# Kernel optimization log

Hardware: AMD Instinct MI355X
Metric: run time of the kernel (lower is better)

The kernel has to match this reference:

```python
import jax, jax.numpy as jnp
import numpy as np

D_MODEL = 1024

def setup_inputs() -> dict:
    key = jax.random.key(0)
    ks = jax.random.split(key, 5)
    d = D_MODEL
    s = 1.0 / np.sqrt(d)
    x = jax.random.normal(ks[0], (4, 4096, d), dtype=jnp.float32)
    qkv_w = jax.random.normal(ks[1], (3 * d, d), dtype=jnp.float32) * s
    qkv_b = jax.random.normal(ks[2], (3 * d,), dtype=jnp.float32) * 0.01
    out_w = jax.random.normal(ks[3], (d, d), dtype=jnp.float32) * s
    out_b = jax.random.normal(ks[4], (d,), dtype=jnp.float32) * 0.01
    return {"x": x, "qkv_w": qkv_w, "qkv_b": qkv_b, "out_w": out_w, "out_b": out_b}

def reference(x, qkv_w, qkv_b, out_w, out_b):
    # x: [b, s, d]; Linear applies x @ W^T + b (torch convention)
    d_model = x.shape[-1]
    qkv = jnp.einsum('bsd,ed->bse', x, qkv_w) + qkv_b  # [b, s, 3d]
    q, k, v = jnp.split(qkv, 3, axis=-1)
    # full-attention branch (chunk_size is None): scores scaled by 1/sqrt(d_model)
    scores = jnp.einsum('bqd,bkd->bqk', q, k) / jnp.sqrt(jnp.float32(d_model))
    attn = jax.nn.softmax(scores, axis=-1)
    attn_out = jnp.einsum('bqk,bkd->bqd', attn, v)
    return jnp.einsum('bsd,ed->bse', attn_out, out_w) + out_b
```

## Files before the change

### kernel.cpp

```cpp
#include <hip/hip_runtime.h>
#include <hip/hip_bf16.h>

typedef __bf16 bf16x8 __attribute__((ext_vector_type(8)));
typedef float f32x4 __attribute__((ext_vector_type(4)));
typedef _Float16 h8 __attribute__((ext_vector_type(8)));
typedef unsigned short u16x8 __attribute__((ext_vector_type(8)));

__device__ inline unsigned short f2b(float x) {
    __hip_bfloat16 h = __float2bfloat16(x);
    return __builtin_bit_cast(unsigned short, h);
}

__device__ inline void gload16(const void* g, void* l) {
    __builtin_amdgcn_global_load_lds(
        (const __attribute__((address_space(1))) unsigned int*)g,
        (__attribute__((address_space(3))) unsigned int*)l, 16, 0, 0);
}

#define BAR  asm volatile("s_barrier" ::: "memory")
#define VMC(N) asm volatile("s_waitcnt vmcnt(" #N ")" ::: "memory")
#define LKM(N) asm volatile("s_waitcnt lgkmcnt(" #N ")")

#define RD_A(BASE, MO)                                                \
    af[0][0] = *(const bf16x8*)((BASE) + (MO) * 1024 + aoff0);        \
    af[0][1] = *(const bf16x8*)((BASE) + (MO) * 1024 + aoff1);        \
    af[1][0] = *(const bf16x8*)((BASE) + ((MO) + 1) * 1024 + aoff0);  \
    af[1][1] = *(const bf16x8*)((BASE) + ((MO) + 1) * 1024 + aoff1);

#define RD_B(BASE)                                                    \
    _Pragma("unroll")                                                 \
    for (int n_ = 0; n_ < 4; ++n_) {                                  \
        bfr[n_][0] = *(const bf16x8*)((BASE) + n_ * 1024 + aoff0);    \
        bfr[n_][1] = *(const bf16x8*)((BASE) + n_ * 1024 + aoff1);    \
    }

#define MFMA_Q(MO)                                                    \
    __builtin_amdgcn_s_setprio(1);                                    \
    _Pragma("unroll")                                                 \
    for (int kk_ = 0; kk_ < 2; ++kk_)                                 \
        _Pragma("unroll")                                             \
        for (int mi_ = 0; mi_ < 2; ++mi_)                             \
            _Pragma("unroll")                                         \
            for (int n_ = 0; n_ < 4; ++n_)                            \
                acc[(MO) + mi_][n_] =                                 \
                    __builtin_amdgcn_mfma_f32_16x16x32_bf16(          \
                        af[mi_][kk_], bfr[n_][kk_],                   \
                        acc[(MO) + mi_][n_], 0, 0, 0);                \
    __builtin_amdgcn_s_setprio(0);

template<int EPI, int SWZ>
__global__ __launch_bounds__(512, 2) void gemm_nt(
    const unsigned short* __restrict__ A, const unsigned short* __restrict__ B,
    long aZ, long bZ, int lda, int ldb, int K,
    const float* __restrict__ bias,
    void* __restrict__ C0, void* __restrict__ C1, void* __restrict__ C2,
    long cZ, int ldc, float scale, int gx, int gy)
{
    __shared__ __attribute__((aligned(16))) unsigned short lds[2][4][8192];

    int wgid;
    if (SWZ) {
        const int nwg = (int)gridDim.x;
        const int bid = (int)blockIdx.x;
        const int qch = nwg >> 3, rch = nwg & 7;
        const int xcd = bid & 7, idx = bid >> 3;
        wgid = (xcd < rch ? xcd * (qch + 1)
                          : rch * (qch + 1) + (xcd - rch) * qch) + idx;
    } else {
        wgid = (int)blockIdx.x;
    }
    const int bx = wgid % gx;
    const int rem = wgid / gx;
    const int by = rem % gy;
    const int z = rem / gy;

    const int t = threadIdx.x;
    const int lane = t & 63, wid = t >> 6;
    const int wr = wid >> 2, wc = wid & 3;
    const int tileM = by * 256, tileN = bx * 256;
    A += (size_t)z * aZ;
    B += (size_t)z * bZ;

    f32x4 acc[8][4] = {};

    const int l4 = lane & 15, qw = lane >> 4, sw = lane & 7;
    const int aoff0 = l4 * 64 + ((qw ^ sw) << 3);
    const int aoff1 = l4 * 64 + (((4 | qw) ^ sw) << 3);

    const unsigned short* aB0 = &lds[0][wr][0];
    const unsigned short* aB1 = &lds[1][wr][0];
    const unsigned short* bB0 = &lds[0][2 + (wc >> 1)][0] + (wc & 1) * 4096;
    const unsigned short* bB1 = &lds[1][2 + (wc >> 1)][0] + (wc & 1) * 4096;

    const int srow = t >> 3;
    const int sg = ((t ^ (t >> 3)) & 7) << 3;
    const unsigned short* Asrc = A + (size_t)(tileM + srow) * lda + sg;
    const unsigned short* Bsrc = B + (size_t)(tileN + srow) * ldb + sg;

    auto stageA = [&](int kt, int h) {
        char* dst = (char*)&lds[kt & 1][h][0] + wid * 1024;
        const unsigned short* s = Asrc + (size_t)(h * 128) * lda + kt * 64;
        gload16(s, dst);
        gload16(s + (size_t)64 * lda, dst + 8192);
    };
    auto stageB = [&](int kt, int h) {
        char* dst = (char*)&lds[kt & 1][2 + h][0] + wid * 1024;
        const unsigned short* s = Bsrc + (size_t)(h * 128) * ldb + kt * 64;
        gload16(s, dst);
        gload16(s + (size_t)64 * ldb, dst + 8192);
    };

    const int NT = K >> 6;
    const int NI = NT >> 1;

    stageA(0, 0); stageA(0, 1); stageB(0, 0); stageB(0, 1);
    stageB(1, 0); stageB(1, 1);
    VMC(4);
    BAR;

    bf16x8 af[2][2], bfr[4][2];

#pragma unroll 1
    for (int i = 0; i < NI; ++i) {
        const int e = 2 * i, o = e + 1;
        const bool more = (i + 1 < NI);

        RD_B(bB0); RD_A(aB0, 0);
        stageA(o, 0);
        LKM(8);
        BAR; LKM(0); MFMA_Q(0); BAR;

        RD_A(aB0, 2);
        stageA(o, 1);
        BAR; LKM(0); MFMA_Q(2); BAR;

        RD_A(aB0, 4);
        if (more) stageB(e + 2, 0);
        BAR; LKM(0); MFMA_Q(4); BAR;

        RD_A(aB0, 6);
        if (more) stageB(e + 2, 1);
        BAR; LKM(0); MFMA_Q(6);
        if (more) VMC(4); else VMC(0);
        BAR;

        RD_B(bB1); RD_A(aB1, 0);
        if (more) stageA(e + 2, 0);
        LKM(8);
        BAR; LKM(0); MFMA_Q(0); BAR;

        RD_A(aB1, 2);
        if (more) stageA(e + 2, 1);
        BAR; LKM(0); MFMA_Q(2); BAR;

        RD_A(aB1, 4);
        if (more) stageB(o + 2, 0);
        BAR; LKM(0); MFMA_Q(4); BAR;

        RD_A(aB1, 6);
        if (more) stageB(o + 2, 1);
        BAR; LKM(0); MFMA_Q(6);
        if (more) { VMC(4); }
        BAR;
    }

    const int lr = lane >> 4, lc = lane & 15;
#pragma unroll
    for (int m = 0; m < 8; ++m) {
#pragma unroll
        for (int n = 0; n < 4; ++n) {
            f32x4 v = acc[m][n];
            const int col = tileN + wc * 64 + n * 16 + lc;
            const int row0 = tileM + wr * 128 + m * 16 + lr * 4;
            if (EPI == 0) {
                const float bv = bias[col];
                if (col < 2048) {
                    unsigned short* dst = (col < 1024) ? (unsigned short*)C0
                                                       : (unsigned short*)C1;
                    const int cc = col & 1023;
#pragma unroll
                    for (int j = 0; j < 4; ++j)
                        dst[(size_t)(row0 + j) * 1024 + cc] = f2b(v[j] + bv);
                } else {
                    const int b = row0 >> 12, s = row0 & 4095;
                    ushort4 h4;
                    h4.x = f2b(v[0] + bv); h4.y = f2b(v[1] + bv);
                    h4.z = f2b(v[2] + bv); h4.w = f2b(v[3] + bv);
                    *(ushort4*)((unsigned short*)C2 +
                                ((size_t)b * 1024 + (col - 2048)) * 4096 + s) = h4;
                }
            } else if (EPI == 1) {
#pragma unroll
                for (int j = 0; j < 4; ++j)
                    ((_Float16*)C0)[(size_t)z * cZ + (size_t)(row0 + j) * ldc + col] =
                        (_Float16)(v[j] * scale);
            } else if (EPI == 2) {
#pragma unroll
                for (int j = 0; j < 4; ++j)
                    ((unsigned short*)C0)[(size_t)z * cZ + (size_t)(row0 + j) * ldc + col] =
                        f2b(v[j]);
            } else {
#pragma unroll
                for (int j = 0; j < 4; ++j)
                    ((float*)C0)[(size_t)(row0 + j) * ldc + col] = v[j] + bias[col];
            }
        }
    }
}

__global__ __launch_bounds__(256) void softmax_rows(unsigned short* __restrict__ sc)
{
    const size_t rowoff = (size_t)blockIdx.x * 4096;
    const int t = threadIdx.x;

    h8 a = *(const h8*)(sc + rowoff + t * 8);
    h8 b = *(const h8*)(sc + rowoff + 2048 + t * 8);
    float v[16];
#pragma unroll
    for (int i = 0; i < 8; ++i) { v[i] = (float)a[i]; v[8 + i] = (float)b[i]; }

    float mx = -1e30f;
#pragma unroll
    for (int i = 0; i < 16; ++i) mx = fmaxf(mx, v[i]);
#pragma unroll
    for (int o = 32; o > 0; o >>= 1) mx = fmaxf(mx, __shfl_xor(mx, o));
    __shared__ float redm[4];
    if ((t & 63) == 0) redm[t >> 6] = mx;
    __syncthreads();
    mx = fmaxf(fmaxf(redm[0], redm[1]), fmaxf(redm[2], redm[3]));

    float sum = 0.f;
#pragma unroll
    for (int i = 0; i < 16; ++i) { v[i] = expf(v[i] - mx); sum += v[i]; }
#pragma unroll
    for (int o = 32; o > 0; o >>= 1) sum += __shfl_xor(sum, o);
    __shared__ float reds[4];
    if ((t & 63) == 0) reds[t >> 6] = sum;
    __syncthreads();
    sum = reds[0] + reds[1] + reds[2] + reds[3];
    const float rs = 1.f / sum;

    u16x8 w0, w1;
#pragma unroll
    for (int i = 0; i < 8; ++i) {
        w0[i] = f2b(v[i] * rs);
        w1[i] = f2b(v[8 + i] * rs);
    }
    *(u16x8*)(sc + rowoff + t * 8) = w0;
    *(u16x8*)(sc + rowoff + 2048 + t * 8) = w1;
}

__global__ __launch_bounds__(256) void cast_bf16(
    const float* __restrict__ in, unsigned short* __restrict__ out, int n4)
{
    const int i = blockIdx.x * 256 + threadIdx.x;
    if (i < n4) {
        float4 f = ((const float4*)in)[i];
        ushort4 o;
        o.x = f2b(f.x); o.y = f2b(f.y); o.z = f2b(f.z); o.w = f2b(f.w);
        ((ushort4*)out)[i] = o;
    }
}

extern "C" void kernel_launch(void* const* d_in, const int* in_sizes, int n_in,
                              void* d_out, int out_size, void* d_ws, size_t ws_size,
                              hipStream_t stream)
{
    const float* x      = (const float*)d_in[0];
    const float* qkv_w  = (const float*)d_in[1];
    const float* qkv_b  = (const float*)d_in[2];
    const float* out_w  = (const float*)d_in[3];
    const float* out_b  = (const float*)d_in[4];
    float* out = (float*)d_out;

    unsigned short* W = (unsigned short*)d_ws;
    const size_t M16 = 16777216;

    if (ws_size >= 236978176ull) {
        unsigned short* sc   = W;
        unsigned short* q    = sc + 67108864;
        unsigned short* kk   = q + M16;
        unsigned short* vT   = kk + M16;
        unsigned short* wo   = vT + M16;
        unsigned short* xb   = sc;
        unsigned short* wqkv = sc + M16;
        unsigned short* ao   = q;

        cast_bf16<<<16384, 256, 0, stream>>>(x, xb, 4194304);
        cast_bf16<<<3072, 256, 0, stream>>>(qkv_w, wqkv, 786432);
        cast_bf16<<<1024, 256, 0, stream>>>(out_w, wo, 262144);

        gemm_nt<0, 0><<<12 * 64, 512, 0, stream>>>(
            xb, wqkv, 0, 0, 1024, 1024, 1024, qkv_b, q, kk, vT, 0, 0, 0.f, 12, 64);

        gemm_nt<1, 0><<<16 * 16 * 4, 512, 0, stream>>>(
            q, kk, 4194304, 4194304, 1024, 1024, 1024, nullptr,
            sc, nullptr, nullptr, 16777216, 4096, 0.03125f, 16, 16);

        softmax_rows<<<16384, 256, 0, stream>>>(sc);

        gemm_nt<2, 1><<<4 * 16 * 4, 512, 0, stream>>>(
            sc, vT, 16777216, 4194304, 4096, 4096, 4096, nullptr,
            ao, nullptr, nullptr, 4194304, 1024, 0.f, 4, 16);

        gemm_nt<3, 0><<<4 * 64, 512, 0, stream>>>(
            ao, wo, 0, 0, 1024, 1024, 1024, out_b,
            out, nullptr, nullptr, 0, 1024, 0.f, 4, 64);
    } else {
        unsigned short* sc   = W;
        unsigned short* q    = sc + M16;
        unsigned short* kk   = q + M16;
        unsigned short* vT   = kk + M16;
        unsigned short* ao   = vT + M16;
        unsigned short* wo   = ao + M16;
        unsigned short* wqkv = wo + 1048576;
        unsigned short* xb   = sc;

        cast_bf16<<<16384, 256, 0, stream>>>(x, xb, 4194304);
        cast_bf16<<<3072, 256, 0, stream>>>(qkv_w, wqkv, 786432);
        cast_bf16<<<1024, 256, 0, stream>>>(out_w, wo, 262144);

        gemm_nt<0, 0><<<12 * 64, 512, 0, stream>>>(
            xb, wqkv, 0, 0, 1024, 1024, 1024, qkv_b, q, kk, vT, 0, 0, 0.f, 12, 64);

        for (int z = 0; z < 4; ++z) {
            const size_t zo = (size_t)z * 4194304;
            gemm_nt<1, 0><<<16 * 16, 512, 0, stream>>>(
                q + zo, kk + zo, 0, 0, 1024, 1024, 1024, nullptr,
                sc, nullptr, nullptr, 0, 4096, 0.03125f, 16, 16);
            softmax_rows<<<4096, 256, 0, stream>>>(sc);
            gemm_nt<2, 1><<<4 * 16, 512, 0, stream>>>(
                sc, vT + zo, 0, 0, 4096, 4096, 4096, nullptr,
                ao + zo, nullptr, nullptr, 0, 1024, 0.f, 4, 16);
        }

        gemm_nt<3, 0><<<4 * 64, 512, 0, stream>>>(
            ao, wo, 0, 0, 1024, 1024, 1024, out_b,
            out, nullptr, nullptr, 0, 1024, 0.f, 4, 64);
    }
}
```

Measured before the change: 473.7 us.

## Restructure GEMM main loop to one barrier per phase and peel the last iteration

Rewrites the double-buffered GEMM main loop so that each phase issues its LDS reads, hits a single barrier, then issues the global-to-LDS prefetch and the MFMAs. This replaces the old pattern of two barriers plus explicit lgkmcnt waits per phase. The final iteration is peeled out so the steady-state loop has no `more` predicates. Stage addressing is also precomputed as base pointers and byte offsets. The aim is to cut barrier and wait overhead and to overlap LDS reads with MFMA work. The cost is relying on compiler-inserted lgkmcnt waits and on barrier placement alone to protect buffer reuse, so correctness depends on that ordering.

New measurement: 442.4 us (median of 2 runs). -6.6%, faster.

```diff
diff --git a/kernel.cpp b/kernel.cpp
--- a/kernel.cpp
+++ b/kernel.cpp
@@ -19,7 +19,6 @@
 
 #define BAR  asm volatile("s_barrier" ::: "memory")
 #define VMC(N) asm volatile("s_waitcnt vmcnt(" #N ")" ::: "memory")
-#define LKM(N) asm volatile("s_waitcnt lgkmcnt(" #N ")")
 
 #define RD_A(BASE, MO)                                                \
     af[0][0] = *(const bf16x8*)((BASE) + (MO) * 1024 + aoff0);        \
@@ -92,20 +91,25 @@
     const unsigned short* bB0 = &lds[0][2 + (wc >> 1)][0] + (wc & 1) * 4096;
     const unsigned short* bB1 = &lds[1][2 + (wc >> 1)][0] + (wc & 1) * 4096;
 
+    char* const ldsA[2] = {(char*)&lds[0][0][0], (char*)&lds[1][0][0]};
+    char* const ldsB[2] = {(char*)&lds[0][2][0], (char*)&lds[1][2][0]};
+
     const int srow = t >> 3;
     const int sg = ((t ^ (t >> 3)) & 7) << 3;
-    const unsigned short* Asrc = A + (size_t)(tileM + srow) * lda + sg;
-    const unsigned short* Bsrc = B + (size_t)(tileN + srow) * ldb + sg;
-
-    auto stageA = [&](int kt, int h) {
-        char* dst = (char*)&lds[kt & 1][h][0] + wid * 1024;
-        const unsigned short* s = Asrc + (size_t)(h * 128) * lda + kt * 64;
+    const unsigned short* Asrc0 = A + (size_t)(tileM + srow) * lda + sg;
+    const unsigned short* Asrc1 = Asrc0 + (size_t)128 * lda;
+    const unsigned short* Bsrc0 = B + (size_t)(tileN + srow) * ldb + sg;
+    const unsigned short* Bsrc1 = Bsrc0 + (size_t)128 * ldb;
+
+    auto stageA = [&](char* Lb, int koff, int h) {
+        char* dst = Lb + h * 16384 + wid * 1024;
+        const unsigned short* s = (h ? Asrc1 : Asrc0) + koff;
         gload16(s, dst);
         gload16(s + (size_t)64 * lda, dst + 8192);
     };
-    auto stageB = [&](int kt, int h) {
-        char* dst = (char*)&lds[kt & 1][2 + h][0] + wid * 1024;
-        const unsigned short* s = Bsrc + (size_t)(h * 128) * ldb + kt * 64;
+    auto stageB = [&](char* Lb, int koff, int h) {
+        char* dst = Lb + h * 16384 + wid * 1024;
+        const unsigned short* s = (h ? Bsrc1 : Bsrc0) + koff;
         gload16(s, dst);
         gload16(s + (size_t)64 * ldb, dst + 8192);
     };
@@ -113,55 +117,74 @@
     const int NT = K >> 6;
     const int NI = NT >> 1;
 
-    stageA(0, 0); stageA(0, 1); stageB(0, 0); stageB(0, 1);
-    stageB(1, 0); stageB(1, 1);
+    stageA(ldsA[0], 0, 0); stageA(ldsA[0], 0, 1);
+    stageB(ldsB[0], 0, 0); stageB(ldsB[0], 0, 1);
+    stageB(ldsB[1], 64, 0); stageB(ldsB[1], 64, 1);
     VMC(4);
     BAR;
 
     bf16x8 af[2][2], bfr[4][2];
 
 #pragma unroll 1
-    for (int i = 0; i < NI; ++i) {
-        const int e = 2 * i, o = e + 1;
-        const bool more = (i + 1 < NI);
+    for (int i = 0; i < NI - 1; ++i) {
+        const int kb = i * 128;
+        const int ko = kb + 64, ke2 = kb + 128, ko2 = kb + 192;
 
         RD_B(bB0); RD_A(aB0, 0);
-        stageA(o, 0);
-        LKM(8);
-        BAR; LKM(0); MFMA_Q(0); BAR;
-
+        BAR; stageA(ldsA[1], ko, 0);
+        MFMA_Q(0)
         RD_A(aB0, 2);
-        stageA(o, 1);
-        BAR; LKM(0); MFMA_Q(2); BAR;
-
+        BAR; stageA(ldsA[1], ko, 1);
+        MFMA_Q(2)
         RD_A(aB0, 4);
-        if (more) stageB(e + 2, 0);
-        BAR; LKM(0); MFMA_Q(4); BAR;
-
+        BAR; stageB(ldsB[0], ke2, 0);
+        MFMA_Q(4)
         RD_A(aB0, 6);
-        if (more) stageB(e + 2, 1);
-        BAR; LKM(0); MFMA_Q(6);
-        if (more) VMC(4); else VMC(0);
-        BAR;
-
+        VMC(2);
+        BAR; stageB(ldsB[0], ke2, 1);
+        MFMA_Q(6)
         RD_B(bB1); RD_A(aB1, 0);
-        if (more) stageA(e + 2, 0);
-        LKM(8);
-        BAR; LKM(0); MFMA_Q(0); BAR;
-
+        BAR; stageA(ldsA[0], ke2, 0);
+        MFMA_Q(0)
         RD_A(aB1, 2);
-        if (more) stageA(e + 2, 1);
-        BAR; LKM(0); MFMA_Q(2); BAR;
-
+        BAR; stageA(ldsA[0], ke2, 1);
+        MFMA_Q(2)
         RD_A(aB1, 4);
-        if (more) stageB(o + 2, 0);
-        BAR; LKM(0); MFMA_Q(4); BAR;
-
+        BAR; stageB(ldsB[1], ko2, 0);
+        MFMA_Q(4)
         RD_A(aB1, 6);
-        if (more) stageB(o + 2, 1);
-        BAR; LKM(0); MFMA_Q(6);
-        if (more) { VMC(4); }
-        BAR;
+        VMC(2);
+        BAR; stageB(ldsB[1], ko2, 1);
+        MFMA_Q(6)
+    }
+
+    {
+        const int ko = (NI - 1) * 128 + 64;
+        RD_B(bB0); RD_A(aB0, 0);
+        BAR; stageA(ldsA[1], ko, 0);
+        MFMA_Q(0)
+        RD_A(aB0, 2);
+        BAR; stageA(ldsA[1], ko, 1);
+        MFMA_Q(2)
+        RD_A(aB0, 4);
+        BAR;
+        MFMA_Q(4)
+        RD_A(aB0, 6);
+        VMC(0);
+        BAR;
+        MFMA_Q(6)
+        RD_B(bB1); RD_A(aB1, 0);
+        BAR;
+        MFMA_Q(0)
+        RD_A(aB1, 2);
+        BAR;
+        MFMA_Q(2)
+        RD_A(aB1, 4);
+        BAR;
+        MFMA_Q(4)
+        RD_A(aB1, 6);
+        BAR;
+        MFMA_Q(6)
     }
 
     const int lr = lane >> 4, lc = lane & 15;
```

## Triple-buffer A tiles in LDS and halve barriers per GEMM quarter-step

Applied to the files above, without the earlier changes.

Replaces the double-buffered LDS layout with three A buffers and two B buffers. The loop is unrolled in groups of three iterations that rotate through the A buffers, and each MFMA quarter-step now needs one barrier instead of two. Global-to-LDS loads for the next tiles are issued right after the barrier, overlapping with the MFMAs, and the explicit lgkmcnt waits are left to the compiler. LDS use grows to 160KB, and the schedule assumes the loop count minus two divides by three, which holds for the K values used here.

Measured after the change: 463.6 us. 1.02x faster.

```diff
diff --git a/kernel.cpp b/kernel.cpp
--- a/kernel.cpp
+++ b/kernel.cpp
@@ -19,7 +19,6 @@
 
 #define BAR  asm volatile("s_barrier" ::: "memory")
 #define VMC(N) asm volatile("s_waitcnt vmcnt(" #N ")" ::: "memory")
-#define LKM(N) asm volatile("s_waitcnt lgkmcnt(" #N ")")
 
 #define RD_A(BASE, MO)                                                \
     af[0][0] = *(const bf16x8*)((BASE) + (MO) * 1024 + aoff0);        \
@@ -56,7 +55,8 @@
     void* __restrict__ C0, void* __restrict__ C1, void* __restrict__ C2,
     long cZ, int ldc, float scale, int gx, int gy)
 {
-    __shared__ __attribute__((aligned(16))) unsigned short lds[2][4][8192];
+    __shared__ __attribute__((aligned(16))) unsigned short ldsA[3][16384];
+    __shared__ __attribute__((aligned(16))) unsigned short ldsB[2][16384];
 
     int wgid;
     if (SWZ) {
@@ -87,25 +87,25 @@
     const int aoff0 = l4 * 64 + ((qw ^ sw) << 3);
     const int aoff1 = l4 * 64 + (((4 | qw) ^ sw) << 3);
 
-    const unsigned short* aB0 = &lds[0][wr][0];
-    const unsigned short* aB1 = &lds[1][wr][0];
-    const unsigned short* bB0 = &lds[0][2 + (wc >> 1)][0] + (wc & 1) * 4096;
-    const unsigned short* bB1 = &lds[1][2 + (wc >> 1)][0] + (wc & 1) * 4096;
+    const unsigned short* bB0 = &ldsB[0][0] + wc * 4096;
+    const unsigned short* bB1 = &ldsB[1][0] + wc * 4096;
 
     const int srow = t >> 3;
     const int sg = ((t ^ (t >> 3)) & 7) << 3;
-    const unsigned short* Asrc = A + (size_t)(tileM + srow) * lda + sg;
-    const unsigned short* Bsrc = B + (size_t)(tileN + srow) * ldb + sg;
-
-    auto stageA = [&](int kt, int h) {
-        char* dst = (char*)&lds[kt & 1][h][0] + wid * 1024;
-        const unsigned short* s = Asrc + (size_t)(h * 128) * lda + kt * 64;
+    const unsigned short* Asrc0 = A + (size_t)(tileM + srow) * lda + sg;
+    const unsigned short* Asrc1 = Asrc0 + (size_t)128 * lda;
+    const unsigned short* Bsrc0 = B + (size_t)(tileN + srow) * ldb + sg;
+    const unsigned short* Bsrc1 = Bsrc0 + (size_t)128 * ldb;
+
+    auto stageAh = [&](int buf, int koff, int h) {
+        char* dst = (char*)&ldsA[buf][0] + h * 16384 + wid * 1024;
+        const unsigned short* s = (h ? Asrc1 : Asrc0) + koff;
         gload16(s, dst);
         gload16(s + (size_t)64 * lda, dst + 8192);
     };
-    auto stageB = [&](int kt, int h) {
-        char* dst = (char*)&lds[kt & 1][2 + h][0] + wid * 1024;
-        const unsigned short* s = Bsrc + (size_t)(h * 128) * ldb + kt * 64;
+    auto stageBh = [&](int buf, int koff, int h) {
+        char* dst = (char*)&ldsB[buf][0] + h * 16384 + wid * 1024;
+        const unsigned short* s = (h ? Bsrc1 : Bsrc0) + koff;
         gload16(s, dst);
         gload16(s + (size_t)64 * ldb, dst + 8192);
     };
@@ -113,56 +113,70 @@
     const int NT = K >> 6;
     const int NI = NT >> 1;
 
-    stageA(0, 0); stageA(0, 1); stageB(0, 0); stageB(0, 1);
-    stageB(1, 0); stageB(1, 1);
-    VMC(4);
+    stageAh(0, 0, 0); stageAh(0, 0, 1);
+    stageBh(0, 0, 0); stageBh(0, 0, 1);
+    stageAh(1, 64, 0); stageAh(1, 64, 1);
+    stageBh(1, 64, 0); stageBh(1, 64, 1);
+    VMC(8);
     BAR;
 
     bf16x8 af[2][2], bfr[4][2];
-
+    int kb = 0;
+
+#define ITER(BE_, BN_, BS_)                                           \
+    {                                                                 \
+        const unsigned short* aE = &ldsA[BE_][0] + wr * 8192;         \
+        const unsigned short* aO = &ldsA[BN_][0] + wr * 8192;         \
+        const int ke2 = kb + 128, ko2 = kb + 192;                     \
+        RD_B(bB0); RD_A(aE, 0);                                       \
+        BAR; stageAh(BS_, ke2, 0); MFMA_Q(0)                          \
+        RD_A(aE, 2);                                                  \
+        BAR; stageAh(BS_, ke2, 1); MFMA_Q(2)                          \
+        RD_A(aE, 4);                                                  \
+        BAR; stageBh(0, ke2, 0); MFMA_Q(4)                            \
+        RD_A(aE, 6); VMC(6);                                          \
+        BAR; stageBh(0, ke2, 1); MFMA_Q(6)                            \
+        RD_B(bB1); RD_A(aO, 0);                                       \
+        BAR; stageAh(BE_, ko2, 0); MFMA_Q(0)                          \
+        RD_A(aO, 2);                                                  \
+        BAR; stageAh(BE_, ko2, 1); MFMA_Q(2)                          \
+        RD_A(aO, 4);                                                  \
+        BAR; stageBh(1, ko2, 0); MFMA_Q(4)                            \
+        RD_A(aO, 6); VMC(6);                                          \
+        BAR; stageBh(1, ko2, 1); MFMA_Q(6)                            \
+        kb += 128;                                                    \
+    }
+
+    const int n3 = (NI - 2) / 3;
 #pragma unroll 1
-    for (int i = 0; i < NI; ++i) {
-        const int e = 2 * i, o = e + 1;
-        const bool more = (i + 1 < NI);
-
-        RD_B(bB0); RD_A(aB0, 0);
-        stageA(o, 0);
-        LKM(8);
-        BAR; LKM(0); MFMA_Q(0); BAR;
-
-        RD_A(aB0, 2);
-        stageA(o, 1);
-        BAR; LKM(0); MFMA_Q(2); BAR;
-
-        RD_A(aB0, 4);
-        if (more) stageB(e + 2, 0);
-        BAR; LKM(0); MFMA_Q(4); BAR;
-
-        RD_A(aB0, 6);
-        if (more) stageB(e + 2, 1);
-        BAR; LKM(0); MFMA_Q(6);
-        if (more) VMC(4); else VMC(0);
-        BAR;
-
-        RD_B(bB1); RD_A(aB1, 0);
-        if (more) stageA(e + 2, 0);
-        LKM(8);
-        BAR; LKM(0); MFMA_Q(0); BAR;
-
-        RD_A(aB1, 2);
-        if (more) stageA(e + 2, 1);
-        BAR; LKM(0); MFMA_Q(2); BAR;
-
-        RD_A(aB1, 4);
-        if (more) stageB(o + 2, 0);
-        BAR; LKM(0); MFMA_Q(4); BAR;
-
-        RD_A(aB1, 6);
-        if (more) stageB(o + 2, 1);
-        BAR; LKM(0); MFMA_Q(6);
-        if (more) { VMC(4); }
-        BAR;
-    }
+    for (int i3 = 0; i3 < n3; ++i3) {
+        ITER(0, 1, 2)
+        ITER(2, 0, 1)
+        ITER(1, 2, 0)
+    }
+    ITER(0, 1, 2)
+
+    {
+        const unsigned short* aE = &ldsA[2][0] + wr * 8192;
+        const unsigned short* aO = &ldsA[0][0] + wr * 8192;
+        RD_B(bB0); RD_A(aE, 0);
+        BAR; MFMA_Q(0)
+        RD_A(aE, 2);
+        BAR; MFMA_Q(2)
+        RD_A(aE, 4);
+        BAR; MFMA_Q(4)
+        RD_A(aE, 6); VMC(0);
+        BAR; MFMA_Q(6)
+        RD_B(bB1); RD_A(aO, 0);
+        BAR; MFMA_Q(0)
+        RD_A(aO, 2);
+        BAR; MFMA_Q(2)
+        RD_A(aO, 4);
+        BAR; MFMA_Q(4)
+        RD_A(aO, 6);
+        BAR; MFMA_Q(6)
+    }
+#undef ITER
 
     const int lr = lane >> 4, lc = lane & 15;
 #pragma unroll
```
